# Kernel optimization log

Measured on AMD Instinct MI355X. Metric: run time of the kernel, lower is better.

The kernel has to match this reference:

```python
import jax, jax.numpy as jnp
import numpy as np

N, K, C, G, B = 65536, 16, 64, 8, 4
PE_IN = 28  # 3 + 1 + 2*4*2 + 1*4*2
EPS = 1e-5
FREQS = (1.0, 2.0, 4.0, 8.0)  # 2 ** linspace(0, 3, 4)


def _bn(x, p):
    # inference-mode BatchNorm1d over last dim; p: [4, d] = (gamma, beta, mean, var)
    return (x - p[2]) * (p[0] / jnp.sqrt(p[3] + EPS)) + p[1]


def setup_inputs() -> dict:
    key = jax.random.key(0)
    ks = iter(jax.random.split(key, 48))

    def nrm(shape, s=0.05):
        return jax.random.normal(next(ks), shape, jnp.float32) * s

    def bnp(d):
        k1, k2, k3, k4 = jax.random.split(next(ks), 4)
        return jnp.stack([
            jax.random.uniform(k1, (d,), jnp.float32, 0.5, 1.5),   # gamma
            jax.random.normal(k2, (d,), jnp.float32) * 0.1,        # beta
            jax.random.normal(k3, (d,), jnp.float32) * 0.1,        # running mean
            jax.random.uniform(k4, (d,), jnp.float32, 0.5, 1.5),   # running var
        ])

    return dict(
        feat=nrm((N, C), 1.0),
        coord=jax.random.normal(next(ks), (N, 3), jnp.float32),
        reference_index=jax.random.randint(next(ks), (N, K), 0, N),
        offset=jnp.array([N // 4, N // 2, 3 * N // 4, N], dtype=jnp.int32),
        Wq=nrm((C, C)), bq=nrm((C,)), bnq=bnp(C),
        Wk=nrm((C, C)), bk=nrm((C,)), bnk=bnp(C),
        Wv=nrm((C, C)), bv=nrm((C,)),
        pe_W1=nrm((PE_IN, C)), pe_b1=nrm((C,)), pe_bn=bnp(C),
        pe_W2=nrm((C, C)), pe_b2=nrm((C,)),
        we_W1=nrm((C, G)), we_b1=nrm((G,)), we_bn=bnp(G),
        we_W2=nrm((G, G)), we_b2=nrm((G,)),
        cg_W1=nrm((3 * C, C)), cg_b1=nrm((C,)), cg_bn=bnp(C),
        cg_W2=nrm((C, G), 0.001), cg_b2=jnp.full((G,), 3.0, jnp.float32),
    )


def reference(feat, coord, reference_index, offset, Wq, bq, bnq, Wk, bk, bnk,
              Wv, bv, pe_W1, pe_b1, pe_bn, pe_W2, pe_b2,
              we_W1, we_b1, we_bn, we_W2, we_b2,
              cg_W1, cg_b1, cg_bn, cg_W2, cg_b2):
    n = feat.shape[0]
    q = jax.nn.relu(_bn(feat @ Wq + bq, bnq))          # [N, C]
    k = jax.nn.relu(_bn(feat @ Wk + bk, bnk))          # [N, C]
    v = feat @ Wv + bv                                 # [N, C]

    idx = reference_index                              # [N, K]; -1 = pad
    idx_safe = jnp.maximum(idx, 0)
    key_feat = k[idx_safe]                             # [N, K, C] gather
    neighbor_xyz = coord[idx_safe]                     # [N, K, 3]
    value_g = v[idx_safe]                              # [N, K, C]

    delta = neighbor_xyz - coord[:, None, :]           # [N, K, 3]
    # Anisotropic Fourier relative position encoding
    x = delta.reshape(-1, 3)
    d_xy, d_z = x[:, :2], x[:, 2:3]
    dist = jnp.linalg.norm(x, axis=1, keepdims=True)
    feats = [x, dist]
    for f in FREQS:
        feats += [jnp.sin(d_xy * (f * np.pi)), jnp.cos(d_xy * (f * np.pi))]
    for f in FREQS:
        feats += [jnp.sin(d_z * (f * np.pi)), jnp.cos(d_z * (f * np.pi))]
    xe = jnp.concatenate(feats, axis=1)                # [N*K, 28]
    rpe = jax.nn.relu(_bn(xe @ pe_W1 + pe_b1, pe_bn)) @ pe_W2 + pe_b2
    rpe = rpe.reshape(n, idx.shape[1], -1)             # [N, K, C]

    relation = key_feat - q[:, None, :] + rpe          # [N, K, C]
    geom_w = jax.nn.relu(_bn(relation @ we_W1 + we_b1, we_bn)) @ we_W2 + we_b2  # [N, K, G]

    neighbor_ctx = q[idx_safe].max(axis=1)             # [N, C]
    seg = jnp.searchsorted(offset, jnp.arange(n), side='right')
    seg_max = jax.ops.segment_max(q, seg, num_segments=offset.shape[0])
    global_ctx = seg_max[seg]                          # [N, C] offset-wise global max pool

    gate_in = jnp.concatenate([q, neighbor_ctx, global_ctx], axis=-1)  # [N, 3C]
    gate = jax.nn.sigmoid(
        jax.nn.relu(_bn(gate_in @ cg_W1 + cg_b1, cg_bn)) @ cg_W2 + cg_b2)  # [N, G]

    attn = jax.nn.softmax(geom_w * gate[:, None, :], axis=1)  # softmax over K
    mask = jnp.sign(idx + 1).astype(attn.dtype)        # [N, K]
    attn = attn * mask[:, :, None]

    vg = value_g.reshape(n, idx.shape[1], G, -1)       # [N, K, G, C//G]
    out = jnp.einsum('nkgi,nkg->ngi', vg, attn)
    return out.reshape(n, -1)
```

## Files before the change

### kernel.cpp

```cpp
#include <hip/hip_runtime.h>
#include <hip/hip_bf16.h>

#define EPSF 1e-5f

typedef __attribute__((ext_vector_type(8))) short short8;
typedef __attribute__((ext_vector_type(4))) float f32x4;

__device__ __forceinline__ int seg_of(int i, int o0, int o1, int o2) {
    return (i >= o0) + (i >= o1) + (i >= o2);
}

__device__ __forceinline__ unsigned short f2bf(float f) {
    unsigned int u = __float_as_uint(f);
    unsigned int r = (u + 0x7fffu + ((u >> 16) & 1u)) >> 16;
    return (unsigned short)r;
}
__device__ __forceinline__ unsigned int pack2bf(float a, float b) {
    return (unsigned int)f2bf(a) | ((unsigned int)f2bf(b) << 16);
}
__device__ __forceinline__ float bflo(unsigned int u) { return __uint_as_float(u << 16); }
__device__ __forceinline__ float bfhi(unsigned int u) { return __uint_as_float(u & 0xffff0000u); }

__device__ __forceinline__ void stage_rows_bf16(const unsigned short* __restrict__ src,
                                                unsigned short* dst, int l) {
    int row = l >> 2, cq = (l & 3) * 16;
    const short8* s = (const short8*)(src + (size_t)row*64 + cq);
    short8* d0 = (short8*)(dst + row*72 + cq);
    d0[0] = s[0];
    d0[1] = s[1];
}

__device__ __forceinline__ void stage_rows_f32(const float* __restrict__ src,
                                               unsigned short* dst, int l) {
    int row = l >> 2, cq = (l & 3) * 16;
    const float4* s = (const float4*)(src + (size_t)row*64 + cq);
    unsigned int* d = (unsigned int*)(dst + row*72 + cq);
    #pragma unroll
    for (int i = 0; i < 4; ++i) {
        float4 f = s[i];
        d[i*2]   = pack2bf(f.x, f.y);
        d[i*2+1] = pack2bf(f.z, f.w);
    }
}

__global__ __launch_bounds__(256) void k_prep(
    const float* __restrict__ pe_W1, const float* __restrict__ pe_b1, const float* __restrict__ pe_bn,
    const float* __restrict__ pe_W2, const float* __restrict__ pe_b2,
    const float* __restrict__ we_W1, const float* __restrict__ we_b1, const float* __restrict__ we_bn,
    const float* __restrict__ we_W2,
    const float* __restrict__ cg_W1, const float* __restrict__ cg_b1, const float* __restrict__ cg_bn,
    const float* __restrict__ cg_W2,
    const float* __restrict__ Wq, const float* __restrict__ bq, const float* __restrict__ bnq,
    const float* __restrict__ Wk, const float* __restrict__ bk, const float* __restrict__ bnk,
    const float* __restrict__ Wv,
    float* __restrict__ peb1f, float* __restrict__ cvecg, float* __restrict__ cgb1f,
    float* __restrict__ biasqF, float* __restrict__ biaskF, float* __restrict__ cgW1cF,
    unsigned short* __restrict__ WqF, unsigned short* __restrict__ WkF, unsigned short* __restrict__ WvF,
    unsigned short* __restrict__ weW1F, unsigned short* __restrict__ cgW1aF,
    unsigned short* __restrict__ cgW1bF, unsigned short* __restrict__ cgW2F,
    unsigned short* __restrict__ W1frag, unsigned short* __restrict__ Wcfrag,
    unsigned short* __restrict__ W2frag)
{
    int t = threadIdx.x;
    __shared__ float sc1[64], csc[64], sqv[64], skv[64], wsc[8], wsh[8];
    __shared__ float sWe[64][8], sWb[8], sWc[64][8];
    if (t < 64) {
        float g = pe_bn[t], b = pe_bn[64+t], m = pe_bn[128+t], v = pe_bn[192+t];
        float s = g / sqrtf(v + EPSF);
        sc1[t] = s; peb1f[t] = pe_b1[t]*s + (b - m*s);
        g = cg_bn[t]; b = cg_bn[64+t]; m = cg_bn[128+t]; v = cg_bn[192+t];
        s = g / sqrtf(v + EPSF);
        csc[t] = s; cgb1f[t] = cg_b1[t]*s + (b - m*s);
        g = bnq[t]; b = bnq[64+t]; m = bnq[128+t]; v = bnq[192+t];
        s = g / sqrtf(v + EPSF);
        sqv[t] = s; biasqF[t] = bq[t]*s + (b - m*s);
        g = bnk[t]; b = bnk[64+t]; m = bnk[128+t]; v = bnk[192+t];
        s = g / sqrtf(v + EPSF);
        skv[t] = s; biaskF[t] = bk[t]*s + (b - m*s);
    }
    if (t < 8) {
        float g = we_bn[t], b = we_bn[8+t], m = we_bn[16+t], v = we_bn[24+t];
        float s = g / sqrtf(v + EPSF);
        wsc[t] = s; wsh[t] = b - m*s;
    }
    __syncthreads();
    for (int u = t; u < 512; u += 256) { int g = u & 7; sWe[u >> 3][g] = we_W1[u] * wsc[g]; }
    if (t < 8) sWb[t] = we_b1[t] * wsc[t] + wsh[t];
    __syncthreads();
    for (int u = t; u < 512; u += 256) {
        int h = u >> 3, g = u & 7;
        float a = 0.f;
        for (int c = 0; c < 64; ++c) a += pe_W2[h*64 + c] * sWe[c][g];
        sWc[h][g] = a;
    }
    if (t < 8) {
        float a = sWb[t];
        for (int c = 0; c < 64; ++c) a += pe_b2[c] * sWe[c][t];
        cvecg[t] = a;
    }
    __syncthreads();
    for (int u = t; u < 4096; u += 256) {
        int tile = u >> 9, l = (u >> 3) & 63, j = u & 7;
        int col = (tile >> 1)*16 + (l & 15);
        int kk  = (tile & 1)*32 + (l >> 4)*8 + j;
        WqF[u]    = f2bf(Wq[kk*64 + col] * sqv[col]);
        WkF[u]    = f2bf(Wk[kk*64 + col] * skv[col]);
        WvF[u]    = f2bf(Wv[kk*64 + col]);
        cgW1aF[u] = f2bf(cg_W1[kk*64 + col] * csc[col]);
        cgW1bF[u] = f2bf(cg_W1[(64 + kk)*64 + col] * csc[col]);
    }
    for (int u = t; u < 1024; u += 256) {
        int tile = u >> 9, l = (u >> 3) & 63, j = u & 7;
        int col = l & 15;
        int kk  = tile*32 + (l >> 4)*8 + j;
        weW1F[u] = (col < 8) ? f2bf(sWe[kk][col]) : 0;
        cgW2F[u] = (col < 8) ? f2bf(cg_W2[kk*8 + col]) : 0;
    }
    for (int u = t; u < 4096; u += 256) {
        int k = u >> 6, c = u & 63;
        cgW1cF[u] = cg_W1[(128 + k)*64 + c] * csc[c];
    }
    {
        int ct = t >> 6, l = t & 63;
        int col = 16*ct + (l & 15), kg = l >> 4;
        #pragma unroll
        for (int j = 0; j < 8; ++j) {
            int k = kg*8 + j;
            float v = (k < 28) ? pe_W1[k*64 + col] * sc1[col] : 0.f;
            W1frag[ct*512 + l*8 + j] = f2bf(v);
        }
    }
    if (t < 128) {
        int kg = t >> 6, l = t & 63, g = l & 15;
        #pragma unroll
        for (int j = 0; j < 8; ++j) {
            int k = kg*32 + (l >> 4)*8 + j;
            float v = (g < 8) ? sWc[k][g] : 0.f;
            Wcfrag[kg*512 + l*8 + j] = f2bf(v);
        }
    }
    if (t < 64) {
        int l = t, g = l & 15;
        #pragma unroll
        for (int j = 0; j < 8; ++j) {
            float v = (l < 16 && g < 8) ? we_W2[j*8 + g] : 0.f;
            W2frag[l*8 + j] = f2bf(v);
        }
    }
}

__global__ __launch_bounds__(256) void k_qkv(
    const float* __restrict__ feat, const int* __restrict__ offs,
    const unsigned short* __restrict__ WqF, const unsigned short* __restrict__ WkF,
    const unsigned short* __restrict__ WvF, const unsigned short* __restrict__ weW1F,
    const float* __restrict__ biasqF, const float* __restrict__ biaskF,
    const float* __restrict__ bv,
    unsigned short* __restrict__ v_bf, unsigned short* __restrict__ q_bf,
    float* __restrict__ kw, float* __restrict__ qw, float* __restrict__ seg_max)
{
    __shared__ unsigned short sF[4][16*72];
    __shared__ unsigned short sQ[4][16*72];
    __shared__ unsigned short sK[4][16*72];
    __shared__ float sSeg[64];

    int t = threadIdx.x, w = t >> 6, l = t & 63;
    int lc = l & 15, lg = l >> 4;
    int rblk = blockIdx.x * 64;
    int r0 = rblk + w * 16;
    int o0 = offs[0], o1 = offs[1], o2 = offs[2];
    bool fast = seg_of(rblk, o0,o1,o2) == seg_of(rblk + 63, o0,o1,o2);

    if (t < 64) sSeg[t] = 0.f;
    __syncthreads();

    stage_rows_f32(feat + (size_t)r0*64, sF[w], l);
    short8 a0 = *(const short8*)(sF[w] + lc*72 + lg*8);
    short8 a1 = *(const short8*)(sF[w] + lc*72 + 32 + lg*8);

    float bqc[4], bkc[4], bvc[4];
    #pragma unroll
    for (int ct = 0; ct < 4; ++ct) {
        bqc[ct] = biasqF[ct*16 + lc];
        bkc[ct] = biaskF[ct*16 + lc];
        bvc[ct] = bv[ct*16 + lc];
    }

    #pragma unroll
    for (int ct = 0; ct < 4; ++ct) {
        f32x4 z = {0.f,0.f,0.f,0.f};
        short8 b0 = *(const short8*)(WqF + (ct*2+0)*512 + l*8);
        short8 b1 = *(const short8*)(WqF + (ct*2+1)*512 + l*8);
        f32x4 c = __builtin_amdgcn_mfma_f32_16x16x32_bf16(a0, b0, z, 0,0,0);
        c = __builtin_amdgcn_mfma_f32_16x16x32_bf16(a1, b1, c, 0,0,0);
        float cmax = 0.f;
        #pragma unroll
        for (int reg = 0; reg < 4; ++reg) {
            float qv = fmaxf(c[reg] + bqc[ct], 0.f);
            sQ[w][(lg*4 + reg)*72 + ct*16 + lc] = f2bf(qv);
            if (fast) cmax = fmaxf(cmax, qv);
            else atomicMax((unsigned int*)&seg_max[seg_of(r0 + lg*4 + reg,o0,o1,o2)*64 + ct*16 + lc],
                           __float_as_uint(qv));
        }
        if (fast) {
            cmax = fmaxf(cmax, __shfl_xor(cmax, 16));
            cmax = fmaxf(cmax, __shfl_xor(cmax, 32));
            if (lg == 0)
                atomicMax((unsigned int*)&sSeg[ct*16 + lc], __float_as_uint(cmax));
        }
    }
    __syncthreads();
    if (fast && t < 64)
        atomicMax((unsigned int*)&seg_max[seg_of(rblk,o0,o1,o2)*64 + t],
                  __float_as_uint(sSeg[t]));

    #pragma unroll
    for (int ct = 0; ct < 4; ++ct) {
        f32x4 z = {0.f,0.f,0.f,0.f};
        short8 b0 = *(const short8*)(WkF + (ct*2+0)*512 + l*8);
        short8 b1 = *(const short8*)(WkF + (ct*2+1)*512 + l*8);
        f32x4 c = __builtin_amdgcn_mfma_f32_16x16x32_bf16(a0, b0, z, 0,0,0);
        c = __builtin_amdgcn_mfma_f32_16x16x32_bf16(a1, b1, c, 0,0,0);
        #pragma unroll
        for (int reg = 0; reg < 4; ++reg)
            sK[w][(lg*4 + reg)*72 + ct*16 + lc] = f2bf(fmaxf(c[reg] + bkc[ct], 0.f));
    }
    #pragma unroll
    for (int ct = 0; ct < 4; ++ct) {
        f32x4 z = {0.f,0.f,0.f,0.f};
        short8 b0 = *(const short8*)(WvF + (ct*2+0)*512 + l*8);
        short8 b1 = *(const short8*)(WvF + (ct*2+1)*512 + l*8);
        f32x4 c = __builtin_amdgcn_mfma_f32_16x16x32_bf16(a0, b0, z, 0,0,0);
        c = __builtin_amdgcn_mfma_f32_16x16x32_bf16(a1, b1, c, 0,0,0);
        #pragma unroll
        for (int reg = 0; reg < 4; ++reg)
            sF[w][(lg*4 + reg)*72 + ct*16 + lc] = f2bf(c[reg] + bvc[ct]);
    }
    {
        short8 wb0 = *(const short8*)(weW1F + l*8);
        short8 wb1 = *(const short8*)(weW1F + 512 + l*8);
        short8 aq0 = *(const short8*)(sQ[w] + lc*72 + lg*8);
        short8 aq1 = *(const short8*)(sQ[w] + lc*72 + 32 + lg*8);
        short8 ak0 = *(const short8*)(sK[w] + lc*72 + lg*8);
        short8 ak1 = *(const short8*)(sK[w] + lc*72 + 32 + lg*8);
        f32x4 z = {0.f,0.f,0.f,0.f};
        f32x4 cq = __builtin_amdgcn_mfma_f32_16x16x32_bf16(aq0, wb0, z, 0,0,0);
        cq = __builtin_amdgcn_mfma_f32_16x16x32_bf16(aq1, wb1, cq, 0,0,0);
        f32x4 ck = __builtin_amdgcn_mfma_f32_16x16x32_bf16(ak0, wb0, z, 0,0,0);
        ck = __builtin_amdgcn_mfma_f32_16x16x32_bf16(ak1, wb1, ck, 0,0,0);
        if (lc < 8) {
            #pragma unroll
            for (int reg = 0; reg < 4; ++reg) {
                qw[(size_t)(r0 + lg*4 + reg)*8 + lc] = cq[reg];
                kw[(size_t)(r0 + lg*4 + reg)*8 + lc] = ck[reg];
            }
        }
    }
    #pragma unroll
    for (int rep = 0; rep < 2; ++rep) {
        int row = (l >> 3) + rep*8;
        int ch = (l & 7) * 8;
        short8 vq = *(const short8*)(sQ[w] + row*72 + ch);
        *(short8*)(q_bf + (size_t)(r0 + row)*64 + ch) = vq;
        short8 vv = *(const short8*)(sF[w] + row*72 + ch);
        *(short8*)(v_bf + (size_t)(r0 + row)*64 + ch) = vv;
    }
}

__global__ __launch_bounds__(256) void k_seg(
    const float* __restrict__ seg_max, const float* __restrict__ cgW1cF,
    const float* __restrict__ cgb1f, float* __restrict__ gseg2)
{
    int t = threadIdx.x;
    int c = t & 63, s = t >> 6;
    float a = cgb1f[c];
    for (int j = 0; j < 64; ++j) a += seg_max[s*64 + j] * cgW1cF[j*64 + c];
    gseg2[s*64 + c] = a;
}

__global__ __launch_bounds__(256, 4) void k_main(
    const float* __restrict__ coord, const int* __restrict__ ridx,
    const unsigned short* __restrict__ v_bf, const unsigned short* __restrict__ q_bf,
    const float* __restrict__ kw, const float* __restrict__ qw,
    const float* __restrict__ peb1f, const float* __restrict__ cvecg,
    const float* __restrict__ we_b2, const float* __restrict__ cg_b2,
    const float* __restrict__ gseg2, const int* __restrict__ offs,
    const unsigned short* __restrict__ W1frag, const unsigned short* __restrict__ Wcfrag,
    const unsigned short* __restrict__ W2frag,
    const unsigned short* __restrict__ cgW1aF, const unsigned short* __restrict__ cgW1bF,
    const unsigned short* __restrict__ cgW2F,
    float* __restrict__ out)
{
    __shared__ __align__(16) unsigned short sA1[256*40];
    __shared__ __align__(16) unsigned short sA2[4][16*72];
    __shared__ __align__(16) unsigned short sU[3456];
    __shared__ float sGate[16][9];
    __shared__ int sIds[256];

    int t = threadIdx.x, w = t >> 6, l = t & 63;
    int lc = l & 15, lg = l >> 4;
    int n0 = blockIdx.x * 16;
    int o0 = offs[0], o1 = offs[1], o2 = offs[2];

    unsigned short* sQg = sU;
    unsigned short* sN  = sU + 1152;
    unsigned short* sHg = sU + 2304;
    unsigned short* sAh2w  = sU + w*128;
    unsigned short* sAttnB = sU + 512;

    int id = ridx[(size_t)n0*16 + t];
    sIds[t] = id;
    int ids = max(id, 0);
    int nself = n0 + (t >> 4);
    {
        float cx = coord[nself*3], cy = coord[nself*3+1], cz = coord[nself*3+2];
        float dx = coord[ids*3]   - cx;
        float dy = coord[ids*3+1] - cy;
        float dz = coord[ids*3+2] - cz;
        float dist = sqrtf(dx*dx + dy*dy + dz*dz);
        unsigned int* row = (unsigned int*)sA1 + t*20;
        row[0] = pack2bf(dx, dy);
        row[1] = pack2bf(dz, dist);
        float sx, cx2, sy, cy2, sz, cz2;
        __sincosf(dx * 3.14159265358979f, &sx, &cx2);
        __sincosf(dy * 3.14159265358979f, &sy, &cy2);
        __sincosf(dz * 3.14159265358979f, &sz, &cz2);
        row[2]  = pack2bf(sx, sy);
        row[3]  = pack2bf(cx2, cy2);
        row[10] = pack2bf(sz, cz2);
        #pragma unroll
        for (int fi = 1; fi < 4; ++fi) {
            float nsx = 2.f*sx*cx2, ncx = fmaf(-2.f*sx, sx, 1.f);
            float nsy = 2.f*sy*cy2, ncy = fmaf(-2.f*sy, sy, 1.f);
            float nsz = 2.f*sz*cz2, ncz = fmaf(-2.f*sz, sz, 1.f);
            row[2 + 2*fi] = pack2bf(nsx, nsy);
            row[3 + 2*fi] = pack2bf(ncx, ncy);
            row[10 + fi]  = pack2bf(nsz, ncz);
            sx = nsx; cx2 = ncx; sy = nsy; cy2 = ncy; sz = nsz; cz2 = ncz;
        }
        row[14] = 0u; row[15] = 0u;
    }
    if (t < 64) stage_rows_bf16(q_bf + (size_t)n0*64, sQg, t);
    __syncthreads();

    {
        int p = t >> 4, s = t & 15;
        const int* ip = &sIds[p*16];
        float m0 = 0.f, m1 = 0.f, m2 = 0.f, m3 = 0.f;
        #pragma unroll
        for (int kb = 0; kb < 16; kb += 4) {
            uint2 u[4];
            #pragma unroll
            for (int j = 0; j < 4; ++j) {
                int idn = max(ip[kb + j], 0);
                u[j] = *(const uint2*)(q_bf + (size_t)idn*64 + s*4);
            }
            #pragma unroll
            for (int j = 0; j < 4; ++j) {
                m0 = fmaxf(m0, bflo(u[j].x)); m1 = fmaxf(m1, bfhi(u[j].x));
                m2 = fmaxf(m2, bflo(u[j].y)); m3 = fmaxf(m3, bfhi(u[j].y));
            }
        }
        unsigned int* d = (unsigned int*)(sN + p*72 + s*4);
        d[0] = pack2bf(m0, m1);
        d[1] = pack2bf(m2, m3);
    }
    __syncthreads();

    {
        short8 a0 = *(const short8*)(sQg + lc*72 + lg*8);
        short8 a1 = *(const short8*)(sQg + lc*72 + 32 + lg*8);
        short8 nv0 = *(const short8*)(sN + lc*72 + lg*8);
        short8 nv1 = *(const short8*)(sN + lc*72 + 32 + lg*8);
        f32x4 c4;
        #pragma unroll
        for (int reg = 0; reg < 4; ++reg)
            c4[reg] = gseg2[seg_of(n0 + lg*4 + reg, o0, o1, o2)*64 + w*16 + lc];
        short8 b0 = *(const short8*)(cgW1aF + (w*2+0)*512 + l*8);
        short8 b1 = *(const short8*)(cgW1aF + (w*2+1)*512 + l*8);
        c4 = __builtin_amdgcn_mfma_f32_16x16x32_bf16(a0, b0, c4, 0,0,0);
        c4 = __builtin_amdgcn_mfma_f32_16x16x32_bf16(a1, b1, c4, 0,0,0);
        short8 b2 = *(const short8*)(cgW1bF + (w*2+0)*512 + l*8);
        short8 b3 = *(const short8*)(cgW1bF + (w*2+1)*512 + l*8);
        c4 = __builtin_amdgcn_mfma_f32_16x16x32_bf16(nv0, b2, c4, 0,0,0);
        c4 = __builtin_amdgcn_mfma_f32_16x16x32_bf16(nv1, b3, c4, 0,0,0);
        #pragma unroll
        for (int reg = 0; reg < 4; ++reg)
            sHg[(lg*4 + reg)*72 + w*16 + lc] = f2bf(fmaxf(c4[reg], 0.f));
    }
    __syncthreads();

    if (w == 0) {
        short8 ah0 = *(const short8*)(sHg + lc*72 + lg*8);
        short8 ah1 = *(const short8*)(sHg + lc*72 + 32 + lg*8);
        short8 w0f = *(const short8*)(cgW2F + l*8);
        short8 w1f = *(const short8*)(cgW2F + 512 + l*8);
        float bg = cg_b2[lc & 7];
        f32x4 cg;
        #pragma unroll
        for (int reg = 0; reg < 4; ++reg) cg[reg] = bg;
        cg = __builtin_amdgcn_mfma_f32_16x16x32_bf16(ah0, w0f, cg, 0,0,0);
        cg = __builtin_amdgcn_mfma_f32_16x16x32_bf16(ah1, w1f, cg, 0,0,0);
        if (lc < 8) {
            #pragma unroll
            for (int reg = 0; reg < 4; ++reg)
                sGate[lg*4 + reg][lc] = 1.f / (1.f + __expf(-cg[reg]));
        }
    }
    __syncthreads();

    int g7 = lc & 7;
    short8 bW1[4], bWc[2], bW2;
    #pragma unroll
    for (int ct = 0; ct < 4; ++ct) bW1[ct] = *(const short8*)(W1frag + ct*512 + l*8);
    bWc[0] = *(const short8*)(Wcfrag + l*8);
    bWc[1] = *(const short8*)(Wcfrag + 512 + l*8);
    bW2 = *(const short8*)(W2frag + l*8);

    float bias1[4];
    #pragma unroll
    for (int ct = 0; ct < 4; ++ct) bias1[ct] = peb1f[16*ct + lc];
    float cvec_g = cvecg[g7];
    float bias3 = we_b2[g7];

    #pragma unroll
    for (int rt = 0; rt < 4; ++rt) {
        int n = n0 + w*4 + rt;
        short8 a1 = *(const short8*)(sA1 + (w*64 + rt*16 + lc)*40 + lg*8);
        f32x4 c1[4];
        #pragma unroll
        for (int ct = 0; ct < 4; ++ct) {
            f32x4 z = {0.f, 0.f, 0.f, 0.f};
            c1[ct] = __builtin_amdgcn_mfma_f32_16x16x32_bf16(a1, bW1[ct], z, 0, 0, 0);
        }
        #pragma unroll
        for (int ct = 0; ct < 4; ++ct) {
            #pragma unroll
            for (int reg = 0; reg < 4; ++reg) {
                float h1 = fmaxf(c1[ct][reg] + bias1[ct], 0.f);
                sA2[w][(lg*4 + reg)*72 + 16*ct + lc] = f2bf(h1);
            }
        }
        int ids_r[4];
        #pragma unroll
        for (int reg = 0; reg < 4; ++reg) ids_r[reg] = sIds[w*64 + rt*16 + lg*4 + reg];
        float qwv = qw[(size_t)n*8 + g7];
        f32x4 c2;
        #pragma unroll
        for (int reg = 0; reg < 4; ++reg)
            c2[reg] = kw[(size_t)max(ids_r[reg],0)*8 + g7] - qwv + cvec_g;
        short8 a20 = *(const short8*)(sA2[w] + lc*72 + lg*8);
        short8 a21 = *(const short8*)(sA2[w] + lc*72 + 32 + lg*8);
        c2 = __builtin_amdgcn_mfma_f32_16x16x32_bf16(a20, bWc[0], c2, 0, 0, 0);
        c2 = __builtin_amdgcn_mfma_f32_16x16x32_bf16(a21, bWc[1], c2, 0, 0, 0);
        if (lc < 8) {
            #pragma unroll
            for (int reg = 0; reg < 4; ++reg)
                sAh2w[(lg*4 + reg)*8 + lc] = f2bf(fmaxf(c2[reg], 0.f));
        }
        short8 a3 = {0,0,0,0,0,0,0,0};
        if (l < 16) a3 = *(const short8*)(sAh2w + lc*8);
        f32x4 c3;
        #pragma unroll
        for (int reg = 0; reg < 4; ++reg) c3[reg] = bias3;
        c3 = __builtin_amdgcn_mfma_f32_16x16x32_bf16(a3, bW2, c3, 0, 0, 0);
        float gv = sGate[w*4 + rt][g7];
        float lgt[4];
        #pragma unroll
        for (int reg = 0; reg < 4; ++reg) lgt[reg] = c3[reg] * gv;
        float m = fmaxf(fmaxf(lgt[0], lgt[1]), fmaxf(lgt[2], lgt[3]));
        m = fmaxf(m, __shfl_xor(m, 16));
        m = fmaxf(m, __shfl_xor(m, 32));
        float e[4], s = 0.f;
        #pragma unroll
        for (int reg = 0; reg < 4; ++reg) { e[reg] = __expf(lgt[reg] - m); s += e[reg]; }
        s += __shfl_xor(s, 16);
        s += __shfl_xor(s, 32);
        float inv = 1.f / s;
        if (lc < 8) {
            #pragma unroll
            for (int reg = 0; reg < 4; ++reg) {
                int idv = ids_r[reg];
                float mf = (idv >= 0) ? 1.f : ((idv == -1) ? 0.f : -1.f);
                sAttnB[((w*4 + rt)*16 + lg*4 + reg)*8 + lc] = f2bf(e[reg] * inv * mf);
            }
        }
    }

    {
        int p = lg, kk = lc;
        int n2 = n0 + w*4 + p;
        float4 o = make_float4(0.f, 0.f, 0.f, 0.f);
        int gh = kk >> 1;
        #pragma unroll
        for (int k2 = 0; k2 < 16; ++k2) {
            int id2 = max(sIds[w*64 + p*16 + k2], 0);
            float a = bflo((unsigned int)sAttnB[((w*4 + p)*16 + k2)*8 + gh]);
            uint2 u = *(const uint2*)(v_bf + (size_t)id2*64 + kk*4);
            o.x += a * bflo(u.x); o.y += a * bfhi(u.x);
            o.z += a * bflo(u.y); o.w += a * bfhi(u.y);
        }
        *(float4*)(out + (size_t)n2*64 + kk*4) = o;
    }
}

extern "C" void kernel_launch(void* const* d_in, const int* in_sizes, int n_in,
                              void* d_out, int out_size, void* d_ws, size_t ws_size,
                              hipStream_t stream)
{
    const float* feat  = (const float*)d_in[0];
    const float* coord = (const float*)d_in[1];
    const int*   ridx  = (const int*)d_in[2];
    const int*   offs  = (const int*)d_in[3];
    const float* Wq = (const float*)d_in[4];  const float* bq = (const float*)d_in[5];  const float* bnq = (const float*)d_in[6];
    const float* Wk = (const float*)d_in[7];  const float* bk = (const float*)d_in[8];  const float* bnk = (const float*)d_in[9];
    const float* Wv = (const float*)d_in[10]; const float* bv = (const float*)d_in[11];
    const float* pe_W1 = (const float*)d_in[12]; const float* pe_b1 = (const float*)d_in[13]; const float* pe_bn = (const float*)d_in[14];
    const float* pe_W2 = (const float*)d_in[15]; const float* pe_b2 = (const float*)d_in[16];
    const float* we_W1 = (const float*)d_in[17]; const float* we_b1 = (const float*)d_in[18]; const float* we_bn = (const float*)d_in[19];
    const float* we_W2 = (const float*)d_in[20]; const float* we_b2 = (const float*)d_in[21];
    const float* cg_W1 = (const float*)d_in[22]; const float* cg_b1 = (const float*)d_in[23]; const float* cg_bn = (const float*)d_in[24];
    const float* cg_W2 = (const float*)d_in[25]; const float* cg_b2 = (const float*)d_in[26];
    float* out = (float*)d_out;
    int N = in_sizes[0] / 64;

    unsigned short* v_bf = (unsigned short*)d_ws;
    unsigned short* q_bf = v_bf + (size_t)N*64;
    float* kwp   = (float*)(q_bf + (size_t)N*64);
    float* qwp   = kwp + (size_t)N*8;
    float* gatep = qwp + (size_t)N*8;
    float* segm  = gatep + (size_t)N*8;
    float* gseg2 = segm + 256;
    float* peb1f = gseg2 + 256;
    float* cvecg = peb1f + 64;
    float* cgb1f = cvecg + 8;
    float* biasqF= cgb1f + 64;
    float* biaskF= biasqF + 64;
    float* pad0  = biaskF + 64;
    float* cgW1cF= pad0 + 56;
    unsigned short* WqF     = (unsigned short*)(cgW1cF + 4096);
    unsigned short* WkF     = WqF + 4096;
    unsigned short* WvF     = WkF + 4096;
    unsigned short* weW1F   = WvF + 4096;
    unsigned short* cgW1aF  = weW1F + 1024;
    unsigned short* cgW1bF  = cgW1aF + 4096;
    unsigned short* cgW2F   = cgW1bF + 4096;
    unsigned short* W1frag  = cgW2F + 1024;
    unsigned short* Wcfrag  = W1frag + 2048;
    unsigned short* W2frag  = Wcfrag + 1024;

    hipMemsetAsync(segm, 0, 256 * sizeof(float), stream);
    k_prep<<<1, 256, 0, stream>>>(pe_W1, pe_b1, pe_bn, pe_W2, pe_b2,
                                  we_W1, we_b1, we_bn, we_W2,
                                  cg_W1, cg_b1, cg_bn, cg_W2,
                                  Wq, bq, bnq, Wk, bk, bnk, Wv,
                                  peb1f, cvecg, cgb1f, biasqF, biaskF, cgW1cF,
                                  WqF, WkF, WvF, weW1F, cgW1aF, cgW1bF, cgW2F,
                                  W1frag, Wcfrag, W2frag);
    k_qkv<<<N/64, 256, 0, stream>>>(feat, offs, WqF, WkF, WvF, weW1F,
                                    biasqF, biaskF, bv,
                                    v_bf, q_bf, kwp, qwp, segm);
    k_seg<<<1, 256, 0, stream>>>(segm, cgW1cF, cgb1f, gseg2);
    k_main<<<N/16, 256, 0, stream>>>(coord, ridx, v_bf, q_bf, kwp, qwp,
                                     peb1f, cvecg, we_b2, cg_b2, gseg2, offs,
                                     W1frag, Wcfrag, W2frag,
                                     cgW1aF, cgW1bF, cgW2F, out);
}
```

Baseline: 105.1 us.

## Fold segment-context GEMV into main kernel, drop memset, shrink LDS for occupancy

Removes the separate k_seg launch and the memset. The segment-max zeroing moves into k_prep, and each k_main block now recomputes the 4x64 global-context projection into shared memory. The per-edge positional-encoding rows stay in registers and are written to a small per-wave LDS tile only when their row is needed. This shrinks LDS from 256x40 to 4x640 shorts, and launch bounds rise from 4 to 6 blocks per CU. The attention weights are also repacked so each thread loads them as two vector reads. The cost is redundant per-block GEMV work (64 loads of seg_max and cgW1cF per thread) and more register pressure from holding xr[16].

```diff
diff --git a/kernel.cpp b/kernel.cpp
--- a/kernel.cpp
+++ b/kernel.cpp
@@ -55,6 +55,7 @@
     const float* __restrict__ Wv,
     float* __restrict__ peb1f, float* __restrict__ cvecg, float* __restrict__ cgb1f,
     float* __restrict__ biasqF, float* __restrict__ biaskF, float* __restrict__ cgW1cF,
+    float* __restrict__ segm,
     unsigned short* __restrict__ WqF, unsigned short* __restrict__ WkF, unsigned short* __restrict__ WvF,
     unsigned short* __restrict__ weW1F, unsigned short* __restrict__ cgW1aF,
     unsigned short* __restrict__ cgW1bF, unsigned short* __restrict__ cgW2F,
@@ -64,6 +65,7 @@
     int t = threadIdx.x;
     __shared__ float sc1[64], csc[64], sqv[64], skv[64], wsc[8], wsh[8];
     __shared__ float sWe[64][8], sWb[8], sWc[64][8];
+    segm[t] = 0.f;
     if (t < 64) {
         float g = pe_bn[t], b = pe_bn[64+t], m = pe_bn[128+t], v = pe_bn[192+t];
         float s = g / sqrtf(v + EPSF);
@@ -266,34 +268,25 @@
     }
 }
 
-__global__ __launch_bounds__(256) void k_seg(
-    const float* __restrict__ seg_max, const float* __restrict__ cgW1cF,
-    const float* __restrict__ cgb1f, float* __restrict__ gseg2)
-{
-    int t = threadIdx.x;
-    int c = t & 63, s = t >> 6;
-    float a = cgb1f[c];
-    for (int j = 0; j < 64; ++j) a += seg_max[s*64 + j] * cgW1cF[j*64 + c];
-    gseg2[s*64 + c] = a;
-}
-
-__global__ __launch_bounds__(256, 4) void k_main(
+__global__ __launch_bounds__(256, 6) void k_main(
     const float* __restrict__ coord, const int* __restrict__ ridx,
     const unsigned short* __restrict__ v_bf, const unsigned short* __restrict__ q_bf,
     const float* __restrict__ kw, const float* __restrict__ qw,
     const float* __restrict__ peb1f, const float* __restrict__ cvecg,
     const float* __restrict__ we_b2, const float* __restrict__ cg_b2,
-    const float* __restrict__ gseg2, const int* __restrict__ offs,
+    const float* __restrict__ seg_max, const float* __restrict__ cgW1cF,
+    const float* __restrict__ cgb1f, const int* __restrict__ offs,
     const unsigned short* __restrict__ W1frag, const unsigned short* __restrict__ Wcfrag,
     const unsigned short* __restrict__ W2frag,
     const unsigned short* __restrict__ cgW1aF, const unsigned short* __restrict__ cgW1bF,
     const unsigned short* __restrict__ cgW2F,
     float* __restrict__ out)
 {
-    __shared__ __align__(16) unsigned short sA1[256*40];
+    __shared__ __align__(16) unsigned short sXe[4*640];
     __shared__ __align__(16) unsigned short sA2[4][16*72];
-    __shared__ __align__(16) unsigned short sU[3456];
+    __shared__ __align__(16) unsigned short sU[3584];
     __shared__ float sGate[16][9];
+    __shared__ float sGseg[4][64];
     __shared__ int sIds[256];
 
     int t = threadIdx.x, w = t >> 6, l = t & 63;
@@ -311,35 +304,42 @@
     sIds[t] = id;
     int ids = max(id, 0);
     int nself = n0 + (t >> 4);
+    unsigned int xr[16];
     {
         float cx = coord[nself*3], cy = coord[nself*3+1], cz = coord[nself*3+2];
         float dx = coord[ids*3]   - cx;
         float dy = coord[ids*3+1] - cy;
         float dz = coord[ids*3+2] - cz;
         float dist = sqrtf(dx*dx + dy*dy + dz*dz);
-        unsigned int* row = (unsigned int*)sA1 + t*20;
-        row[0] = pack2bf(dx, dy);
-        row[1] = pack2bf(dz, dist);
+        xr[0] = pack2bf(dx, dy);
+        xr[1] = pack2bf(dz, dist);
         float sx, cx2, sy, cy2, sz, cz2;
         __sincosf(dx * 3.14159265358979f, &sx, &cx2);
         __sincosf(dy * 3.14159265358979f, &sy, &cy2);
         __sincosf(dz * 3.14159265358979f, &sz, &cz2);
-        row[2]  = pack2bf(sx, sy);
-        row[3]  = pack2bf(cx2, cy2);
-        row[10] = pack2bf(sz, cz2);
+        xr[2]  = pack2bf(sx, sy);
+        xr[3]  = pack2bf(cx2, cy2);
+        xr[10] = pack2bf(sz, cz2);
         #pragma unroll
         for (int fi = 1; fi < 4; ++fi) {
             float nsx = 2.f*sx*cx2, ncx = fmaf(-2.f*sx, sx, 1.f);
             float nsy = 2.f*sy*cy2, ncy = fmaf(-2.f*sy, sy, 1.f);
             float nsz = 2.f*sz*cz2, ncz = fmaf(-2.f*sz, sz, 1.f);
-            row[2 + 2*fi] = pack2bf(nsx, nsy);
-            row[3 + 2*fi] = pack2bf(ncx, ncy);
-            row[10 + fi]  = pack2bf(nsz, ncz);
+            xr[2 + 2*fi] = pack2bf(nsx, nsy);
+            xr[3 + 2*fi] = pack2bf(ncx, ncy);
+            xr[10 + fi]  = pack2bf(nsz, ncz);
             sx = nsx; cx2 = ncx; sy = nsy; cy2 = ncy; sz = nsz; cz2 = ncz;
         }
-        row[14] = 0u; row[15] = 0u;
+        xr[14] = 0u; xr[15] = 0u;
     }
     if (t < 64) stage_rows_bf16(q_bf + (size_t)n0*64, sQg, t);
+    {
+        float a = cgb1f[l];
+        #pragma unroll 8
+        for (int j = 0; j < 64; ++j)
+            a += seg_max[w*64 + j] * cgW1cF[j*64 + l];
+        sGseg[w][l] = a;
+    }
     __syncthreads();
 
     {
@@ -374,7 +374,7 @@
         f32x4 c4;
         #pragma unroll
         for (int reg = 0; reg < 4; ++reg)
-            c4[reg] = gseg2[seg_of(n0 + lg*4 + reg, o0, o1, o2)*64 + w*16 + lc];
+            c4[reg] = sGseg[seg_of(n0 + lg*4 + reg, o0, o1, o2)][w*16 + lc];
         short8 b0 = *(const short8*)(cgW1aF + (w*2+0)*512 + l*8);
         short8 b1 = *(const short8*)(cgW1aF + (w*2+1)*512 + l*8);
         c4 = __builtin_amdgcn_mfma_f32_16x16x32_bf16(a0, b0, c4, 0,0,0);
@@ -421,11 +421,17 @@
     for (int ct = 0; ct < 4; ++ct) bias1[ct] = peb1f[16*ct + lc];
     float cvec_g = cvecg[g7];
     float bias3 = we_b2[g7];
+    unsigned short* sXw = sXe + w*640;
 
     #pragma unroll
     for (int rt = 0; rt < 4; ++rt) {
         int n = n0 + w*4 + rt;
-        short8 a1 = *(const short8*)(sA1 + (w*64 + rt*16 + lc)*40 + lg*8);
+        if (lg == rt) {
+            unsigned int* dst = (unsigned int*)(sXw + lc*40);
+            #pragma unroll
+            for (int i = 0; i < 16; ++i) dst[i] = xr[i];
+        }
+        short8 a1 = *(const short8*)(sXw + lc*40 + lg*8);
         f32x4 c1[4];
         #pragma unroll
         for (int ct = 0; ct < 4; ++ct) {
@@ -477,24 +483,31 @@
         s += __shfl_xor(s, 32);
         float inv = 1.f / s;
         if (lc < 8) {
+            float av[4];
             #pragma unroll
             for (int reg = 0; reg < 4; ++reg) {
                 int idv = ids_r[reg];
                 float mf = (idv >= 0) ? 1.f : ((idv == -1) ? 0.f : -1.f);
-                sAttnB[((w*4 + rt)*16 + lg*4 + reg)*8 + lc] = f2bf(e[reg] * inv * mf);
+                av[reg] = e[reg] * inv * mf;
             }
+            unsigned int* d = (unsigned int*)(sAttnB + ((w*4 + rt)*8 + lc)*24 + lg*4);
+            d[0] = pack2bf(av[0], av[1]);
+            d[1] = pack2bf(av[2], av[3]);
         }
     }
 
     {
         int p = lg, kk = lc;
         int n2 = n0 + w*4 + p;
+        const unsigned short* ab = sAttnB + ((w*4 + p)*8 + (kk >> 1))*24;
+        short8 aa0 = *(const short8*)(ab);
+        short8 aa1 = *(const short8*)(ab + 8);
         float4 o = make_float4(0.f, 0.f, 0.f, 0.f);
-        int gh = kk >> 1;
         #pragma unroll
         for (int k2 = 0; k2 < 16; ++k2) {
             int id2 = max(sIds[w*64 + p*16 + k2], 0);
-            float a = bflo((unsigned int)sAttnB[((w*4 + p)*16 + k2)*8 + gh]);
+            unsigned short ar = (k2 < 8) ? (unsigned short)aa0[k2] : (unsigned short)aa1[k2-8];
+            float a = bflo((unsigned int)ar);
             uint2 u = *(const uint2*)(v_bf + (size_t)id2*64 + kk*4);
             o.x += a * bflo(u.x); o.y += a * bfhi(u.x);
             o.z += a * bflo(u.y); o.w += a * bfhi(u.y);
@@ -527,10 +540,8 @@
     unsigned short* q_bf = v_bf + (size_t)N*64;
     float* kwp   = (float*)(q_bf + (size_t)N*64);
     float* qwp   = kwp + (size_t)N*8;
-    float* gatep = qwp + (size_t)N*8;
-    float* segm  = gatep + (size_t)N*8;
-    float* gseg2 = segm + 256;
-    float* peb1f = gseg2 + 256;
+    float* segm  = qwp + (size_t)N*8;
+    float* peb1f = segm + 256;
     float* cvecg = peb1f + 64;
     float* cgb1f = cvecg + 8;
     float* biasqF= cgb1f + 64;
@@ -548,20 +559,19 @@
     unsigned short* Wcfrag  = W1frag + 2048;
     unsigned short* W2frag  = Wcfrag + 1024;
 
-    hipMemsetAsync(segm, 0, 256 * sizeof(float), stream);
     k_prep<<<1, 256, 0, stream>>>(pe_W1, pe_b1, pe_bn, pe_W2, pe_b2,
                                   we_W1, we_b1, we_bn, we_W2,
                                   cg_W1, cg_b1, cg_bn, cg_W2,
                                   Wq, bq, bnq, Wk, bk, bnk, Wv,
-                                  peb1f, cvecg, cgb1f, biasqF, biaskF, cgW1cF,
+                                  peb1f, cvecg, cgb1f, biasqF, biaskF, cgW1cF, segm,
                                   WqF, WkF, WvF, weW1F, cgW1aF, cgW1bF, cgW2F,
                                   W1frag, Wcfrag, W2frag);
     k_qkv<<<N/64, 256, 0, stream>>>(feat, offs, WqF, WkF, WvF, weW1F,
                                     biasqF, biaskF, bv,
                                     v_bf, q_bf, kwp, qwp, segm);
-    k_seg<<<1, 256, 0, stream>>>(segm, cgW1cF, cgb1f, gseg2);
     k_main<<<N/16, 256, 0, stream>>>(coord, ridx, v_bf, q_bf, kwp, qwp,
-                                     peb1f, cvecg, we_b2, cg_b2, gseg2, offs,
+                                     peb1f, cvecg, we_b2, cg_b2,
+                                     segm, cgW1cF, cgb1f, offs,
                                      W1frag, Wcfrag, W2frag,
                                      cgW1aF, cgW1bF, cgW2F, out);
 }
```

Measured after the change: 135.2 us. 1.29x slower.
